# Optimization experiments

Hardware: AMD Instinct MI355X
Metric: run time of the kernel (lower is better)

## Reference

```python
import jax, jax.numpy as jnp
import numpy as np

B, N, K = 8, 2048, 4          # graphs per batch, nodes per graph, knn k
IN_CH, HID, C = 16, 128, 64   # in_channels, GCN hidden, n_clusters
E = 262144                    # input edges


def gcn_conv(x, src, dst, W, b):
    """PyG GCNConv: self-loops + symmetric normalization + linear."""
    n = x.shape[0]
    xw = x @ W
    loop = jnp.arange(n)
    s2 = jnp.concatenate([src, loop])
    d2 = jnp.concatenate([dst, loop])
    deg = jax.ops.segment_sum(jnp.ones(s2.shape[0], x.dtype), d2, num_segments=n)
    dis = jax.lax.rsqrt(deg)  # deg >= 1 thanks to self loops
    norm = dis[s2] * dis[d2]
    return jax.ops.segment_sum(xw[s2] * norm[:, None], d2, num_segments=n) + b


def knn_edges(coords):
    """knn_graph(k=K, loop=False) per graph; edges neighbor->node (source_to_target)."""
    c = coords.reshape(B, N, 3)
    d2 = jnp.sum((c[:, :, None, :] - c[:, None, :, :]) ** 2, -1)  # [B,N,N]
    d2 = d2 + jnp.eye(N, dtype=c.dtype) * jnp.asarray(1e10, c.dtype)  # exclude self
    _, idx = jax.lax.top_k(-d2, K)  # [B,N,K] local neighbor indices
    offs = (jnp.arange(B) * N)[:, None, None]
    src = (idx + offs).reshape(-1)
    dst = (jnp.broadcast_to(jnp.arange(N)[None, :, None], (B, N, K)) + offs).reshape(-1)
    return src, dst


def dmon_pool(x, adj, Wp, bp):
    """PyG DMoNPooling (eval mode, mask all-true since graphs are equal-sized)."""
    s = jax.nn.softmax(x @ Wp + bp, axis=-1)              # [B,N,C]
    out = jax.nn.selu(jnp.einsum('bnc,bnf->bcf', s, x))   # [B,C,F]
    out_adj = jnp.einsum('bnc,bnm,bmd->bcd', s, adj, s)   # [B,C,C]
    deg = adj.sum(1)                                      # column sums, [B,N]
    m = deg.sum(-1) / 2                                   # [B]
    ca = jnp.einsum('bnc,bn->bc', s, deg)                 # [B,C]
    normalizer = ca[:, :, None] * ca[:, None, :] / (2 * m)[:, None, None]
    spectral = (-jnp.trace(out_adj - normalizer, axis1=1, axis2=2) / (2 * m)).mean()
    ss = jnp.einsum('bnc,bnd->bcd', s, s)
    ss_fro = jnp.linalg.norm(ss, axis=(1, 2), keepdims=True)
    i_norm = jnp.sqrt(jnp.asarray(C, x.dtype))            # ||I_C||_F
    i_s = jnp.eye(C, dtype=x.dtype)
    ortho = jnp.linalg.norm(ss / ss_fro - i_s / i_norm, axis=(1, 2)).mean()
    cluster = (jnp.linalg.norm(s.sum(1), axis=1) / N * i_norm - 1).mean()
    return s, out, spectral, ortho, cluster


def forward(x, edge_src, edge_dst, W1, b1, W2, b2, Wp, bp):
    h = jax.nn.relu(gcn_conv(x, edge_src, edge_dst, W1, b1))
    src2, dst2 = knn_edges(h[:, :3])                      # dynamic graph on dims [0,1,2]
    h = jax.nn.relu(gcn_conv(h, src2, dst2, W2, b2))
    xd = h.reshape(B, N, HID)                             # to_dense_batch (equal-size graphs)
    g = edge_src // N                                     # to_dense_adj on ORIGINAL edges
    adj = jnp.zeros((B, N, N), x.dtype).at[g, edge_src % N, edge_dst % N].add(1.0)
    s, out, sp, o, cl = dmon_pool(xd, adj, Wp, bp)
    return jax.nn.log_softmax(out, axis=-1), sp + o + cl, s


def setup_inputs():
    key = jax.random.key(0)
    ks = jax.random.split(key, 8)
    x = jax.random.normal(ks[0], (B * N, IN_CH), jnp.float32)
    g = jax.random.randint(ks[1], (E,), 0, B)
    edge_src = (g * N + jax.random.randint(ks[2], (E,), 0, N)).astype(jnp.int32)
    edge_dst = (g * N + jax.random.randint(ks[3], (E,), 0, N)).astype(jnp.int32)
    batch = jnp.repeat(jnp.arange(B, dtype=jnp.int32), N)
    W1 = jax.random.normal(ks[4], (IN_CH, HID), jnp.float32) / np.sqrt(IN_CH)
    b1 = jnp.zeros((HID,), jnp.float32)
    W2 = jax.random.normal(ks[5], (HID, HID), jnp.float32) / np.sqrt(HID)
    b2 = jnp.zeros((HID,), jnp.float32)
    Wp = jax.random.normal(ks[6], (HID, C), jnp.float32) / np.sqrt(HID)
    bp = jnp.zeros((C,), jnp.float32)
    return {"x": x, "edge_src": edge_src, "edge_dst": edge_dst, "batch": batch,
            "W1": W1, "b1": b1, "W2": W2, "b2": b2, "Wp": Wp, "bp": bp}


def reference(x, edge_src, edge_dst, batch, W1, b1, W2, b2, Wp, bp):
    del batch  # graphs are equal-sized contiguous blocks of N nodes
    return forward(x, edge_src, edge_dst, W1, b1, W2, b2, Wp, bp)
```

## Files before the change

### kernel.cpp

```cpp
#include <hip/hip_runtime.h>
#include <math.h>

#define BGR 8
#define NN 2048
#define KNN 4
#define INCH 16
#define HID 128
#define CL 64
#define NE 262144
#define NT (BGR*NN)

#define OFF_DEG   0
#define OFF_AGG1  16384
#define OFF_H1    278528
#define OFF_NBR   2375680
#define OFF_AGG2  2441216
#define OFF_H2    4538368
#define OFF_TR    6733824
#define OFF_CA    6733832
#define OFF_SSUM  6734344
#define OFF_MS    6734856

__global__ void k_init(float* ws, float* small, float* loss) {
  int i = blockIdx.x * 256 + threadIdx.x;
  if (i < 278528) ws[i] = 0.f;
  int j = i - 278528;
  if (j >= 0 && j < 1040) small[j] = 0.f;
  if (i == 0) loss[0] = 0.f;
}

__global__ void k_deg(const int* __restrict__ dst, float* __restrict__ deg) {
  int e = blockIdx.x * 256 + threadIdx.x;
  if (e < NE) atomicAdd(&deg[dst[e]], 1.0f);
}

__global__ void k_scatter1(const int* __restrict__ src, const int* __restrict__ dst,
                           const float* __restrict__ x, const float* __restrict__ deg,
                           float* __restrict__ agg1) {
  int t = blockIdx.x * 256 + threadIdx.x;
  int e = t >> 4, c = t & 15;
  if (e >= NE) return;
  int s = src[e], d = dst[e];
  float ds = 1.0f / sqrtf(deg[s] + 1.0f);
  atomicAdd(&agg1[d * INCH + c], x[s * INCH + c] * ds);
}

__global__ __launch_bounds__(256) void k_gemm1(const float* __restrict__ agg1,
    const float* __restrict__ x, const float* __restrict__ deg,
    const float* __restrict__ W1, const float* __restrict__ b1, float* __restrict__ h1) {
  __shared__ float a1[16][17];
  __shared__ float w[INCH * HID];
  int tid = threadIdx.x;
  for (int i = tid; i < INCH * HID / 4; i += 256) ((float4*)w)[i] = ((const float4*)W1)[i];
  int nl = tid >> 4, ch = tid & 15;
  int n = blockIdx.x * 16 + nl;
  float dn = 1.0f / sqrtf(deg[n] + 1.0f);
  a1[nl][ch] = (agg1[n * INCH + ch] + x[n * INCH + ch] * dn) * dn;
  __syncthreads();
  int j = tid & 127;
  int ng = (tid >> 7) * 8;
#pragma unroll
  for (int u = 0; u < 8; u++) {
    int node = ng + u;
    float s = b1[j];
#pragma unroll
    for (int c2 = 0; c2 < INCH; c2++) s += a1[node][c2] * w[c2 * HID + j];
    h1[(size_t)(blockIdx.x * 16 + node) * HID + j] = fmaxf(s, 0.f);
  }
}

__global__ __launch_bounds__(1024) void k_knn(const float* __restrict__ h1, int* __restrict__ nbr) {
  __shared__ float4 c4[NN];
  int g = blockIdx.y, tid = threadIdx.x;
  for (int i = tid; i < NN; i += 1024)
    c4[i] = *(const float4*)(h1 + (size_t)(g * NN + i) * HID);
  __syncthreads();
  int wid = tid >> 6, lane = tid & 63;
  int row0 = blockIdx.x * 32 + wid * 2;
  float mx[2], my[2], mz[2];
#pragma unroll
  for (int r = 0; r < 2; r++) { float4 m = c4[row0 + r]; mx[r] = m.x; my[r] = m.y; mz[r] = m.z; }
  unsigned t0[2], t1[2], t2[2], t3[2];
#pragma unroll
  for (int r = 0; r < 2; r++) { t0[r] = t1[r] = t2[r] = t3[r] = 0xFFFFFFFFu; }
#pragma unroll 4
  for (int i = 0; i < 32; i++) {
    int j = i * 64 + lane;
    float4 p = c4[j];
#pragma unroll
    for (int r = 0; r < 2; r++) {
      float dx = p.x - mx[r], dy = p.y - my[r], dz = p.z - mz[r];
      float d2 = dx * dx + dy * dy + dz * dz;
      unsigned k = (__float_as_uint(d2) & 0xFFFFFFE0u) | (unsigned)i;
      if (j == row0 + r) k = 0xFFFFFFFFu;
      unsigned M0 = max(t0[r], k); t0[r] = min(t0[r], k);
      unsigned M1 = max(t1[r], M0); t1[r] = min(t1[r], M0);
      unsigned M2 = max(t2[r], M1); t2[r] = min(t2[r], M1);
      t3[r] = min(t3[r], M2);
    }
  }
#pragma unroll
  for (int r = 0; r < 2; r++) {
    unsigned a0 = t0[r], a1 = t1[r], a2 = t2[r], a3 = t3[r];
    int res[4];
#pragma unroll
    for (int k = 0; k < 4; k++) {
      int cj = (int)((a0 & 31u) << 6) | lane;
      unsigned wd = a0; int wj = cj;
#pragma unroll
      for (int off = 32; off; off >>= 1) {
        unsigned od = (unsigned)__shfl_xor((int)wd, off, 64);
        int oj = __shfl_xor(wj, off, 64);
        bool take = (od < wd) || (od == wd && oj < wj);
        wd = take ? od : wd; wj = take ? oj : wj;
      }
      res[k] = wj;
      bool pop = (cj == wj);
      a0 = pop ? a1 : a0; a1 = pop ? a2 : a1; a2 = pop ? a3 : a2;
      a3 = pop ? 0xFFFFFFFFu : a3;
    }
    if (lane == 0) {
      int node = g * NN + row0 + r;
      ((int4*)nbr)[node] = make_int4(g * NN + res[0], g * NN + res[1],
                                     g * NN + res[2], g * NN + res[3]);
    }
  }
}

__global__ __launch_bounds__(256) void k_gemm2f(const float* __restrict__ h1,
    const int* __restrict__ nbr, const float* __restrict__ W2,
    const float* __restrict__ b2, float* __restrict__ h2) {
  __shared__ float At[64][17];
  __shared__ float Bt[16 * 128];
  int tid = threadIdx.x;
  int rbase = blockIdx.x * 64;
  int r = tid >> 2, q = tid & 3;
  int4 nb = ((const int4*)nbr)[rbase + r];
  const float4* h4 = (const float4*)h1;
  size_t r0 = (size_t)(rbase + r) * 32, rx = (size_t)nb.x * 32, ry = (size_t)nb.y * 32,
         rz = (size_t)nb.z * 32, rw = (size_t)nb.w * 32;
  int rg = tid >> 5;
  int cg = (tid & 31) * 4;
  float acc[8][4];
#pragma unroll
  for (int i = 0; i < 8; i++)
#pragma unroll
    for (int j = 0; j < 4; j++) acc[i][j] = 0.f;
  for (int k0 = 0; k0 < HID; k0 += 16) {
    {
      int q4 = (k0 >> 2) + q;
      float4 a = h4[r0 + q4], bx = h4[rx + q4], by = h4[ry + q4],
             bz = h4[rz + q4], bw = h4[rw + q4];
      int kk = q * 4;
      At[r][kk]     = (a.x + bx.x + by.x + bz.x + bw.x) * 0.2f;
      At[r][kk + 1] = (a.y + bx.y + by.y + bz.y + bw.y) * 0.2f;
      At[r][kk + 2] = (a.z + bx.z + by.z + bz.z + bw.z) * 0.2f;
      At[r][kk + 3] = (a.w + bx.w + by.w + bz.w + bw.w) * 0.2f;
    }
    {
      int kk = tid >> 5;
      int cc = (tid & 31) * 4;
      *(float4*)&Bt[kk * 128 + cc] = *(const float4*)&W2[(k0 + kk) * HID + cc];
      *(float4*)&Bt[(kk + 8) * 128 + cc] = *(const float4*)&W2[(k0 + kk + 8) * HID + cc];
    }
    __syncthreads();
#pragma unroll
    for (int kk = 0; kk < 16; kk++) {
      float4 bv = *(const float4*)&Bt[kk * 128 + cg];
#pragma unroll
      for (int i = 0; i < 8; i++) {
        float av = At[rg * 8 + i][kk];
        acc[i][0] += av * bv.x; acc[i][1] += av * bv.y;
        acc[i][2] += av * bv.z; acc[i][3] += av * bv.w;
      }
    }
    __syncthreads();
  }
#pragma unroll
  for (int i = 0; i < 8; i++) {
    int rr = rbase + rg * 8 + i;
#pragma unroll
    for (int j = 0; j < 4; j++) {
      float v = acc[i][j] + b2[cg + j];
      h2[(size_t)rr * HID + cg + j] = fmaxf(v, 0.f);
    }
  }
}

__global__ __launch_bounds__(256) void k_s(const float* __restrict__ h2,
    const float* __restrict__ Wp, const float* __restrict__ bp, float* __restrict__ s_out) {
  int tid = threadIdx.x, wid = tid >> 6, lane = tid & 63;
  float w[HID];
#pragma unroll
  for (int k = 0; k < HID; k++) w[k] = Wp[k * CL + lane];
  float bpv = bp[lane];
  int nbase = blockIdx.x * 32 + wid * 8;
  for (int u = 0; u < 8; u++) {
    int n = nbase + u;
    const float4* hp = (const float4*)(h2 + (size_t)n * HID);
    float acc = bpv;
#pragma unroll
    for (int k4 = 0; k4 < 32; k4++) {
      float4 h = hp[k4];
      acc += h.x * w[k4 * 4] + h.y * w[k4 * 4 + 1] + h.z * w[k4 * 4 + 2] + h.w * w[k4 * 4 + 3];
    }
    float m = acc;
    for (int off = 32; off; off >>= 1) m = fmaxf(m, __shfl_xor(m, off, 64));
    float e = expf(acc - m);
    float sum = e;
    for (int off = 32; off; off >>= 1) sum += __shfl_xor(sum, off, 64);
    s_out[(size_t)n * CL + lane] = e / sum;
  }
}

__global__ __launch_bounds__(256) void k_dmon_trace(const float* __restrict__ s,
    const float* __restrict__ h2, const float* __restrict__ deg,
    float* __restrict__ part_pool, float* __restrict__ part_ss,
    float* __restrict__ ca, float* __restrict__ ssum, float* __restrict__ msum,
    const int* __restrict__ src, const int* __restrict__ dst, float* __restrict__ tr) {
  __shared__ float st[64 * 64];
  __shared__ float ht[64 * 128];
  __shared__ float dt[64];
  __shared__ float red[256];
  __shared__ float bins[8];
  int tid = threadIdx.x;
  if (blockIdx.x < 256) {
    int b = blockIdx.x >> 5, sl = blockIdx.x & 31;
    int nb = sl * 64;
    const float* sp = s + ((size_t)b * NN + nb) * CL;
    const float* hp = h2 + ((size_t)b * NN + nb) * HID;
    for (int i = tid; i < 64 * 64 / 4; i += 256) ((float4*)st)[i] = ((const float4*)sp)[i];
    for (int i = tid; i < 64 * 128 / 4; i += 256) ((float4*)ht)[i] = ((const float4*)hp)[i];
    if (tid < 64) dt[tid] = deg[b * NN + nb + tid];
    __syncthreads();
    int c = tid & 63;
    int fg = (tid >> 6) * 32;
    float acc[32];
#pragma unroll
    for (int i = 0; i < 32; i++) acc[i] = 0.f;
    for (int n = 0; n < 64; n++) {
      float a = st[n * 64 + c];
#pragma unroll
      for (int i = 0; i < 32; i++) acc[i] += a * ht[n * 128 + fg + i];
    }
    float* pp = part_pool + ((size_t)(b * 32 + sl)) * 8192 + c * 128 + fg;
#pragma unroll
    for (int i = 0; i < 32; i += 4)
      *(float4*)&pp[i] = make_float4(acc[i], acc[i + 1], acc[i + 2], acc[i + 3]);
    int dg = (tid >> 6) * 16;
    float sacc[16];
#pragma unroll
    for (int i = 0; i < 16; i++) sacc[i] = 0.f;
    for (int n = 0; n < 64; n++) {
      float a = st[n * 64 + c];
#pragma unroll
      for (int i = 0; i < 16; i++) sacc[i] += a * st[n * 64 + dg + i];
    }
    float* ps = part_ss + ((size_t)(b * 32 + sl)) * 4096 + c * 64 + dg;
#pragma unroll
    for (int i = 0; i < 16; i += 4)
      *(float4*)&ps[i] = make_float4(sacc[i], sacc[i + 1], sacc[i + 2], sacc[i + 3]);
    int q = tid >> 6;
    float a_ss = 0, a_ca = 0, a_m = 0;
    for (int n = q; n < 64; n += 4) {
      float sv = st[n * 64 + c];
      float dv = dt[n];
      a_ss += sv; a_ca += sv * dv;
      if (c == 0) a_m += dv;
    }
    red[tid] = a_ss; __syncthreads();
    if (q == 0) atomicAdd(&ssum[b * CL + c], red[c] + red[64 + c] + red[128 + c] + red[192 + c]);
    __syncthreads();
    red[tid] = a_ca; __syncthreads();
    if (q == 0) atomicAdd(&ca[b * CL + c], red[c] + red[64 + c] + red[128 + c] + red[192 + c]);
    __syncthreads();
    red[tid] = (c == 0) ? a_m : 0.f; __syncthreads();
    if (tid == 0) atomicAdd(&msum[b], red[0] + red[64] + red[128] + red[192]);
  } else {
    if (tid < 8) bins[tid] = 0.f;
    __syncthreads();
    int sub = tid & 15;
    int grp = ((blockIdx.x - 256) * 256 + tid) >> 4;
    const float4* s4 = (const float4*)s;
    for (int e = grp; e < NE; e += 8192) {
      int se = src[e], de = dst[e];
      float4 a = s4[se * 16 + sub];
      float4 b = s4[de * 16 + sub];
      float v = a.x * b.x + a.y * b.y + a.z * b.z + a.w * b.w;
      v += __shfl_xor(v, 1, 64);
      v += __shfl_xor(v, 2, 64);
      v += __shfl_xor(v, 4, 64);
      v += __shfl_xor(v, 8, 64);
      if (sub == 0) atomicAdd(&bins[se >> 11], v);
    }
    __syncthreads();
    if (tid < 8) atomicAdd(&tr[tid], bins[tid]);
  }
}

__global__ __launch_bounds__(256) void k_final(const float* __restrict__ part_pool,
    const float* __restrict__ part_ss, const float* __restrict__ ca,
    const float* __restrict__ ssum, const float* __restrict__ msum,
    const float* __restrict__ tr, float* __restrict__ out, float* __restrict__ outs) {
  int tid = threadIdx.x;
  if (blockIdx.x < 256) {
    __shared__ float r[4], r2[4];
    int half = tid >> 7, f = tid & 127;
    int row = blockIdx.x * 2 + half;
    int wid = tid >> 6;
    const float* p = part_pool + (size_t)(row >> 6) * 32 * 8192 + (row & 63) * 128 + f;
    float v = 0.f;
#pragma unroll
    for (int sl = 0; sl < 32; sl++) v += p[sl * 8192];
    const float scale = 1.0507009873554805f, alpha = 1.6732632423543772f;
    v = scale * (v > 0.f ? v : alpha * expm1f(v));
    float m = v;
    for (int off = 32; off; off >>= 1) m = fmaxf(m, __shfl_xor(m, off, 64));
    if ((tid & 63) == 0) r[wid] = m;
    __syncthreads();
    m = fmaxf(r[half * 2], r[half * 2 + 1]);
    float e = expf(v - m);
    float sum = e;
    for (int off = 32; off; off >>= 1) sum += __shfl_xor(sum, off, 64);
    if ((tid & 63) == 0) r2[wid] = sum;
    __syncthreads();
    sum = r2[half * 2] + r2[half * 2 + 1];
    out[(size_t)row * HID + f] = v - m - logf(sum);
  } else {
    __shared__ float ssb[4096];
    __shared__ float red[256];
    int b = blockIdx.x - 256;
    float loc = 0.f;
    for (int idx = tid; idx < 4096; idx += 256) {
      const float* p = part_ss + (size_t)b * 32 * 4096 + idx;
      float v = 0.f;
#pragma unroll
      for (int sl = 0; sl < 32; sl++) v += p[sl * 4096];
      ssb[idx] = v;
      loc += v * v;
    }
    red[tid] = loc; __syncthreads();
    for (int s2 = 128; s2; s2 >>= 1) { if (tid < s2) red[tid] += red[tid + s2]; __syncthreads(); }
    float fro = sqrtf(red[0]);
    __syncthreads();
    loc = 0.f;
    for (int i = tid; i < 4096; i += 256) {
      float v = ssb[i] / fro - (((i % 65) == 0) ? 0.125f : 0.f);
      loc += v * v;
    }
    red[tid] = loc; __syncthreads();
    for (int s2 = 128; s2; s2 >>= 1) { if (tid < s2) red[tid] += red[tid + s2]; __syncthreads(); }
    float ortho_b = sqrtf(red[0]);
    __syncthreads();
    loc = 0.f;
    if (tid < 64) { float v = ca[b * 64 + tid]; loc = v * v; }
    red[tid] = loc; __syncthreads();
    for (int s2 = 128; s2; s2 >>= 1) { if (tid < s2) red[tid] += red[tid + s2]; __syncthreads(); }
    float caSq = red[0];
    __syncthreads();
    loc = 0.f;
    if (tid < 64) { float v = ssum[b * 64 + tid]; loc = v * v; }
    red[tid] = loc; __syncthreads();
    for (int s2 = 128; s2; s2 >>= 1) { if (tid < s2) red[tid] += red[tid + s2]; __syncthreads(); }
    float ssumSq = red[0];
    __syncthreads();
    if (tid == 0) {
      float m2 = msum[b];
      float spectral_b = -(tr[b] - caSq / m2) / m2;
      float cluster_b = sqrtf(ssumSq) / 2048.0f * 8.0f - 1.0f;
      atomicAdd(&outs[0], (spectral_b + ortho_b + cluster_b) * 0.125f);
    }
  }
}

extern "C" void kernel_launch(void* const* d_in, const int* in_sizes, int n_in,
                              void* d_out, int out_size, void* d_ws, size_t ws_size,
                              hipStream_t stream) {
  (void)in_sizes; (void)n_in; (void)out_size; (void)ws_size;
  const float* x   = (const float*)d_in[0];
  const int* esrc  = (const int*)d_in[1];
  const int* edst  = (const int*)d_in[2];
  const float* W1  = (const float*)d_in[4];
  const float* b1  = (const float*)d_in[5];
  const float* W2  = (const float*)d_in[6];
  const float* b2  = (const float*)d_in[7];
  const float* Wp  = (const float*)d_in[8];
  const float* bp  = (const float*)d_in[9];
  float* out = (float*)d_out;
  float* ws  = (float*)d_ws;

  float* deg   = ws + OFF_DEG;
  float* agg1  = ws + OFF_AGG1;
  float* h1    = ws + OFF_H1;
  int*   nbr   = (int*)(ws + OFF_NBR);
  float* h2    = ws + OFF_H2;
  float* tr    = ws + OFF_TR;
  float* ca    = ws + OFF_CA;
  float* ssum  = ws + OFF_SSUM;
  float* msum  = ws + OFF_MS;
  float* part_pool = ws + OFF_H1;
  float* part_ss   = ws + OFF_AGG2;
  float* s_out = out + 65537;

  k_init<<<1093, 256, 0, stream>>>(ws, ws + OFF_TR, out + 65536);
  k_deg<<<NE / 256, 256, 0, stream>>>(edst, deg);
  k_scatter1<<<NE * 16 / 256, 256, 0, stream>>>(esrc, edst, x, deg, agg1);
  k_gemm1<<<NT / 16, 256, 0, stream>>>(agg1, x, deg, W1, b1, h1);
  k_knn<<<dim3(64, 8), 1024, 0, stream>>>(h1, nbr);
  k_gemm2f<<<NT / 64, 256, 0, stream>>>(h1, nbr, W2, b2, h2);
  k_s<<<NT / 32, 256, 0, stream>>>(h2, Wp, bp, s_out);
  k_dmon_trace<<<768, 256, 0, stream>>>(s_out, h2, deg, part_pool, part_ss,
                                        ca, ssum, msum, esrc, edst, tr);
  k_final<<<264, 256, 0, stream>>>(part_pool, part_ss, ca, ssum, msum, tr,
                                   out, out + 65536);
}
```

Before: 236.8 us.

## Replicate scatter targets, compact knn coords, retile gemm2, vectorize init

The first GCN scatter now spreads atomics across four replicated accumulation buffers chosen by block index, and gemm1 sums the four copies. This is meant to reduce atomic contention, at the cost of zeroing and reading four times as much buffer. gemm1 also writes a compact 4-float coordinate array so the knn kernel loads 16 bytes per node instead of striding through the full hidden rows. gemm2 is retiled to 32 rows by 32-deep k chunks to double the block count, and the init kernel now zeroes with float4 stores. The workspace offsets are reshuffled to fit the larger buffers.

```diff
diff --git a/kernel.cpp b/kernel.cpp
--- a/kernel.cpp
+++ b/kernel.cpp
@@ -12,19 +12,20 @@
 
 #define OFF_DEG   0
 #define OFF_AGG1  16384
-#define OFF_H1    278528
-#define OFF_NBR   2375680
-#define OFF_AGG2  2441216
-#define OFF_H2    4538368
-#define OFF_TR    6733824
-#define OFF_CA    6733832
-#define OFF_SSUM  6734344
-#define OFF_MS    6734856
-
-__global__ void k_init(float* ws, float* small, float* loss) {
+#define OFF_H1    1064960
+#define OFF_NBR   3162112
+#define OFF_SS    3227648
+#define OFF_H2    4276224
+#define OFF_TR    6373376
+#define OFF_CA    6373384
+#define OFF_SSUM  6373896
+#define OFF_MS    6374408
+#define OFF_H1C   6374416
+
+__global__ void k_init(float4* ws4, float* small, float* loss) {
   int i = blockIdx.x * 256 + threadIdx.x;
-  if (i < 278528) ws[i] = 0.f;
-  int j = i - 278528;
+  if (i < 266240) ws4[i] = make_float4(0.f, 0.f, 0.f, 0.f);
+  int j = i - 266240;
   if (j >= 0 && j < 1040) small[j] = 0.f;
   if (i == 0) loss[0] = 0.f;
 }
@@ -42,12 +43,14 @@
   if (e >= NE) return;
   int s = src[e], d = dst[e];
   float ds = 1.0f / sqrtf(deg[s] + 1.0f);
-  atomicAdd(&agg1[d * INCH + c], x[s * INCH + c] * ds);
+  float* tgt = agg1 + ((blockIdx.x & 3) * 262144);
+  atomicAdd(&tgt[d * INCH + c], x[s * INCH + c] * ds);
 }
 
 __global__ __launch_bounds__(256) void k_gemm1(const float* __restrict__ agg1,
     const float* __restrict__ x, const float* __restrict__ deg,
-    const float* __restrict__ W1, const float* __restrict__ b1, float* __restrict__ h1) {
+    const float* __restrict__ W1, const float* __restrict__ b1,
+    float* __restrict__ h1, float* __restrict__ h1c) {
   __shared__ float a1[16][17];
   __shared__ float w[INCH * HID];
   int tid = threadIdx.x;
@@ -55,7 +58,9 @@
   int nl = tid >> 4, ch = tid & 15;
   int n = blockIdx.x * 16 + nl;
   float dn = 1.0f / sqrtf(deg[n] + 1.0f);
-  a1[nl][ch] = (agg1[n * INCH + ch] + x[n * INCH + ch] * dn) * dn;
+  int idx = n * INCH + ch;
+  float ag = agg1[idx] + agg1[262144 + idx] + agg1[524288 + idx] + agg1[786432 + idx];
+  a1[nl][ch] = (ag + x[idx] * dn) * dn;
   __syncthreads();
   int j = tid & 127;
   int ng = (tid >> 7) * 8;
@@ -65,15 +70,17 @@
     float s = b1[j];
 #pragma unroll
     for (int c2 = 0; c2 < INCH; c2++) s += a1[node][c2] * w[c2 * HID + j];
-    h1[(size_t)(blockIdx.x * 16 + node) * HID + j] = fmaxf(s, 0.f);
-  }
-}
-
-__global__ __launch_bounds__(1024) void k_knn(const float* __restrict__ h1, int* __restrict__ nbr) {
+    float v = fmaxf(s, 0.f);
+    h1[(size_t)(blockIdx.x * 16 + node) * HID + j] = v;
+    if (j < 4) h1c[(size_t)(blockIdx.x * 16 + node) * 4 + j] = v;
+  }
+}
+
+__global__ __launch_bounds__(1024) void k_knn(const float* __restrict__ h1c, int* __restrict__ nbr) {
   __shared__ float4 c4[NN];
   int g = blockIdx.y, tid = threadIdx.x;
-  for (int i = tid; i < NN; i += 1024)
-    c4[i] = *(const float4*)(h1 + (size_t)(g * NN + i) * HID);
+  const float4* src4 = (const float4*)h1c + (size_t)g * NN;
+  for (int i = tid; i < NN; i += 1024) c4[i] = src4[i];
   __syncthreads();
   int wid = tid >> 6, lane = tid & 63;
   int row0 = blockIdx.x * 32 + wid * 2;
@@ -130,46 +137,45 @@
 __global__ __launch_bounds__(256) void k_gemm2f(const float* __restrict__ h1,
     const int* __restrict__ nbr, const float* __restrict__ W2,
     const float* __restrict__ b2, float* __restrict__ h2) {
-  __shared__ float At[64][17];
-  __shared__ float Bt[16 * 128];
+  __shared__ float At[32][33];
+  __shared__ float Bt[32 * 128];
   int tid = threadIdx.x;
-  int rbase = blockIdx.x * 64;
-  int r = tid >> 2, q = tid & 3;
+  int rbase = blockIdx.x * 32;
+  int r = tid >> 3, q = tid & 7;
   int4 nb = ((const int4*)nbr)[rbase + r];
   const float4* h4 = (const float4*)h1;
   size_t r0 = (size_t)(rbase + r) * 32, rx = (size_t)nb.x * 32, ry = (size_t)nb.y * 32,
          rz = (size_t)nb.z * 32, rw = (size_t)nb.w * 32;
   int rg = tid >> 5;
   int cg = (tid & 31) * 4;
-  float acc[8][4];
-#pragma unroll
-  for (int i = 0; i < 8; i++)
+  float acc[4][4];
+#pragma unroll
+  for (int i = 0; i < 4; i++)
 #pragma unroll
     for (int j = 0; j < 4; j++) acc[i][j] = 0.f;
-  for (int k0 = 0; k0 < HID; k0 += 16) {
+  int kk = tid >> 5;
+  int cc = (tid & 31) * 4;
+  for (int k0 = 0; k0 < HID; k0 += 32) {
     {
       int q4 = (k0 >> 2) + q;
       float4 a = h4[r0 + q4], bx = h4[rx + q4], by = h4[ry + q4],
              bz = h4[rz + q4], bw = h4[rw + q4];
-      int kk = q * 4;
-      At[r][kk]     = (a.x + bx.x + by.x + bz.x + bw.x) * 0.2f;
-      At[r][kk + 1] = (a.y + bx.y + by.y + bz.y + bw.y) * 0.2f;
-      At[r][kk + 2] = (a.z + bx.z + by.z + bz.z + bw.z) * 0.2f;
-      At[r][kk + 3] = (a.w + bx.w + by.w + bz.w + bw.w) * 0.2f;
-    }
-    {
-      int kk = tid >> 5;
-      int cc = (tid & 31) * 4;
-      *(float4*)&Bt[kk * 128 + cc] = *(const float4*)&W2[(k0 + kk) * HID + cc];
-      *(float4*)&Bt[(kk + 8) * 128 + cc] = *(const float4*)&W2[(k0 + kk + 8) * HID + cc];
-    }
-    __syncthreads();
-#pragma unroll
-    for (int kk = 0; kk < 16; kk++) {
-      float4 bv = *(const float4*)&Bt[kk * 128 + cg];
-#pragma unroll
-      for (int i = 0; i < 8; i++) {
-        float av = At[rg * 8 + i][kk];
+      int k = q * 4;
+      At[r][k]     = (a.x + bx.x + by.x + bz.x + bw.x) * 0.2f;
+      At[r][k + 1] = (a.y + bx.y + by.y + bz.y + bw.y) * 0.2f;
+      At[r][k + 2] = (a.z + bx.z + by.z + bz.z + bw.z) * 0.2f;
+      At[r][k + 3] = (a.w + bx.w + by.w + bz.w + bw.w) * 0.2f;
+    }
+#pragma unroll
+    for (int u = 0; u < 4; u++)
+      *(float4*)&Bt[(kk + u * 8) * 128 + cc] = *(const float4*)&W2[(k0 + kk + u * 8) * HID + cc];
+    __syncthreads();
+#pragma unroll
+    for (int k2 = 0; k2 < 32; k2++) {
+      float4 bv = *(const float4*)&Bt[k2 * 128 + cg];
+#pragma unroll
+      for (int i = 0; i < 4; i++) {
+        float av = At[rg * 4 + i][k2];
         acc[i][0] += av * bv.x; acc[i][1] += av * bv.y;
         acc[i][2] += av * bv.z; acc[i][3] += av * bv.w;
       }
@@ -177,8 +183,8 @@
     __syncthreads();
   }
 #pragma unroll
-  for (int i = 0; i < 8; i++) {
-    int rr = rbase + rg * 8 + i;
+  for (int i = 0; i < 4; i++) {
+    int rr = rbase + rg * 4 + i;
 #pragma unroll
     for (int j = 0; j < 4; j++) {
       float v = acc[i][j] + b2[cg + j];
@@ -398,16 +404,17 @@
   float* ca    = ws + OFF_CA;
   float* ssum  = ws + OFF_SSUM;
   float* msum  = ws + OFF_MS;
+  float* h1c   = ws + OFF_H1C;
   float* part_pool = ws + OFF_H1;
-  float* part_ss   = ws + OFF_AGG2;
+  float* part_ss   = ws + OFF_SS;
   float* s_out = out + 65537;
 
-  k_init<<<1093, 256, 0, stream>>>(ws, ws + OFF_TR, out + 65536);
+  k_init<<<1045, 256, 0, stream>>>((float4*)ws, ws + OFF_TR, out + 65536);
   k_deg<<<NE / 256, 256, 0, stream>>>(edst, deg);
   k_scatter1<<<NE * 16 / 256, 256, 0, stream>>>(esrc, edst, x, deg, agg1);
-  k_gemm1<<<NT / 16, 256, 0, stream>>>(agg1, x, deg, W1, b1, h1);
-  k_knn<<<dim3(64, 8), 1024, 0, stream>>>(h1, nbr);
-  k_gemm2f<<<NT / 64, 256, 0, stream>>>(h1, nbr, W2, b2, h2);
+  k_gemm1<<<NT / 16, 256, 0, stream>>>(agg1, x, deg, W1, b1, h1, h1c);
+  k_knn<<<dim3(64, 8), 1024, 0, stream>>>(h1c, nbr);
+  k_gemm2f<<<NT / 32, 256, 0, stream>>>(h1, nbr, W2, b2, h2);
   k_s<<<NT / 32, 256, 0, stream>>>(h2, Wp, bp, s_out);
   k_dmon_trace<<<768, 256, 0, stream>>>(s_out, h2, deg, part_pool, part_ss,
                                         ca, ssum, msum, esrc, edst, tr);
```

After: 229.0 us. -3.3%, faster.
